# Optimization experiments

Measured on AMD Instinct MI355X. Metric: run time of the kernel, lower is better.

The kernel has to match this reference:

```python
import jax, jax.numpy as jnp
import numpy as np

NUM_HEADS = 8
EPS = 1e-3

N_TOKENS = 32768
DIM = 256
N_WIN = 128
WIN = N_TOKENS // N_WIN  # 256 tokens per window


def setup_inputs() -> dict:
    key = jax.random.key(0)
    ks = jax.random.split(key, 4)
    x = jax.random.normal(ks[0], (N_TOKENS, DIM), dtype=jnp.float32)
    # torch nn.Linear weights are [out_features, in_features]
    w_qkv = jax.random.normal(ks[1], (3 * DIM, DIM), dtype=jnp.float32) * (DIM ** -0.5)
    w_proj = jax.random.normal(ks[2], (DIM, DIM), dtype=jnp.float32) * (DIM ** -0.5)
    b_proj = jnp.zeros((DIM,), dtype=jnp.float32)
    batch_win_inds = (jnp.arange(N_TOKENS) // WIN).astype(jnp.int64)
    offsets = (jnp.arange(N_WIN) * WIN).astype(jnp.int64)
    counts = jnp.full((N_WIN,), WIN, dtype=jnp.int64)
    return {"x": x, "w_qkv": w_qkv, "w_proj": w_proj, "b_proj": b_proj,
            "offsets": offsets, "counts": counts, "batch_win_inds": batch_win_inds}


def reference(x, w_qkv, w_proj, b_proj, offsets, counts, batch_win_inds):
    N, C = x.shape
    H = NUM_HEADS
    hd = C // H
    W = counts.shape[0]  # number of windows (static)

    qkv = x @ w_qkv.T                      # [N, 3C]
    q, k, v = jnp.split(qkv, 3, axis=-1)   # each [N, C]
    q = jax.nn.relu(q.reshape(N, H, hd))   # [N, H, hd]
    k = jax.nn.relu(k.reshape(N, H, hd))
    v = v.reshape(N, H, hd)

    seg = batch_win_inds.astype(jnp.int32)
    # per-window KV state: kv[w] = sum_{i in w} k_i^T v_i   -> [W, H, hd, hd]
    kv = jax.ops.segment_sum(jnp.einsum('nhc,nhd->nhcd', k, v), seg, num_segments=W)
    # per-window key sum for normalizer                      -> [W, H, hd]
    s = jax.ops.segment_sum(k, seg, num_segments=W)

    y = jnp.einsum('nhc,nhcd->nhd', q, kv[seg])              # [N, H, hd]
    z = jnp.sum(s[seg] * q, axis=-1, keepdims=True)          # [N, H, 1]
    y = y / (z + EPS)

    y = y.reshape(N, C) @ w_proj.T + b_proj                  # [N, C]
    return y
```

## Files before the change

### kernel.cpp

```cpp
#include <hip/hip_runtime.h>

typedef __bf16 bf16_t;
typedef bf16_t bf16x8 __attribute__((ext_vector_type(8)));
typedef bf16_t bf16x4 __attribute__((ext_vector_type(4)));
typedef float f32x4 __attribute__((ext_vector_type(4)));

#define M_TOK 32768
#define NWIN 128
#define WIN  256

typedef __attribute__((address_space(3))) void* as3p;
typedef const __attribute__((address_space(1))) void* as1p;

__device__ __forceinline__ void gll16(const void* g, void* l) {
    __builtin_amdgcn_global_load_lds((as1p)g, (as3p)l, 16, 0, 0);
}

__device__ __forceinline__ bf16x8 cvt8(f32x4 a, f32x4 b) {
    bf16x8 o;
    o[0] = (bf16_t)a[0]; o[1] = (bf16_t)a[1]; o[2] = (bf16_t)a[2]; o[3] = (bf16_t)a[3];
    o[4] = (bf16_t)b[0]; o[5] = (bf16_t)b[1]; o[6] = (bf16_t)b[2]; o[7] = (bf16_t)b[3];
    return o;
}

__global__ __launch_bounds__(256) void wconv(
    const float* __restrict__ wq, const float* __restrict__ wp,
    bf16_t* __restrict__ wqb, bf16_t* __restrict__ wpb)
{
    int i4 = (blockIdx.x * 256 + threadIdx.x) * 4;
    const float* s; bf16_t* dst; int idx;
    if (i4 < 196608) { s = wq; dst = wqb; idx = i4; }
    else             { s = wp; dst = wpb; idx = i4 - 196608; }
    f32x4 v = *(const f32x4*)(s + idx);
    bf16x4 o;
    o[0] = (bf16_t)v[0]; o[1] = (bf16_t)v[1]; o[2] = (bf16_t)v[2]; o[3] = (bf16_t)v[3];
    *(bf16x4*)(dst + idx) = o;
}

__global__ __launch_bounds__(256) void gemm1_qkv(
    const float* __restrict__ X,
    const bf16_t* __restrict__ Wb,
    bf16_t* __restrict__ Qg,
    bf16_t* __restrict__ KTg,
    bf16_t* __restrict__ VTg)
{
    __shared__ float  As[4][128][16];
    __shared__ bf16_t Bs[2][128][32];

    const int tid = threadIdx.x;
    const int lane = tid & 63;
    const int wv = tid >> 6;
    const int wm = wv >> 1, wn = wv & 1;
    const int id = blockIdx.x;
    const int sg = id / 48, wsub = id % 48;
    const int m0 = (sg * 8 + (wsub & 7)) * 128;
    const int n0 = (wsub >> 3) * 128;
    const int r = lane & 15, q = lane >> 4;
    const int srow = lane >> 2;

    f32x4 acc[4][4] = {};

    for (int kc = 0; kc < 256; kc += 64) {
#pragma unroll
        for (int p = 0; p < 4; ++p)
#pragma unroll
            for (int g = 0; g < 2; ++g) {
                const int rb = wv * 32 + g * 16;
                gll16(X + (size_t)(m0 + rb + srow) * 256 + kc + p * 16 + (lane & 3) * 4,
                      &As[p][rb][0]);
            }
#pragma unroll
        for (int p = 0; p < 2; ++p)
#pragma unroll
            for (int g = 0; g < 2; ++g) {
                const int rb = wv * 32 + g * 16;
                gll16(Wb + (size_t)(n0 + rb + srow) * 256 + kc + p * 32 + (lane & 3) * 8,
                      &Bs[p][rb][0]);
            }
        __syncthreads();

#pragma unroll
        for (int kk = 0; kk < 64; kk += 32) {
            const int kq = kk + q * 8;
            const int pA = kq >> 4, offA = kq & 15;
            const int pB = kk >> 5;
            bf16x8 a[4], b[4];
#pragma unroll
            for (int i = 0; i < 4; ++i) {
                f32x4 lo = *(const f32x4*)&As[pA][wm * 64 + i * 16 + r][offA];
                f32x4 hi = *(const f32x4*)&As[pA][wm * 64 + i * 16 + r][offA + 4];
                a[i] = cvt8(lo, hi);
            }
#pragma unroll
            for (int j = 0; j < 4; ++j)
                b[j] = *(const bf16x8*)&Bs[pB][wn * 64 + j * 16 + r][q * 8];
#pragma unroll
            for (int i = 0; i < 4; ++i)
#pragma unroll
                for (int j = 0; j < 4; ++j)
                    acc[i][j] = __builtin_amdgcn_mfma_f32_16x16x32_bf16(b[j], a[i], acc[i][j], 0, 0, 0);
        }
        __syncthreads();
    }

#pragma unroll
    for (int i = 0; i < 4; ++i) {
        const int rowg = m0 + wm * 64 + i * 16 + r;
#pragma unroll
        for (int j = 0; j < 4; ++j) {
            const int nbase = n0 + wn * 64 + j * 16 + q * 4;
            if (nbase < 256) {
                const int hq = nbase >> 5, d = nbase & 31;
                bf16x4 o;
#pragma unroll
                for (int reg = 0; reg < 4; ++reg)
                    o[reg] = (bf16_t)fmaxf(acc[i][j][reg], 0.0f);
                *(bf16x4*)&Qg[((size_t)hq * M_TOK + rowg) * 32 + d] = o;
            } else if (nbase < 512) {
                const int hh = (nbase >> 5) - 8, c0 = nbase & 31;
#pragma unroll
                for (int reg = 0; reg < 4; ++reg)
                    KTg[((size_t)hh * 32 + c0 + reg) * M_TOK + rowg] =
                        (bf16_t)fmaxf(acc[i][j][reg], 0.0f);
            } else {
                const int hh = (nbase >> 5) - 16, c0 = nbase & 31;
#pragma unroll
                for (int reg = 0; reg < 4; ++reg)
                    VTg[((size_t)hh * 32 + c0 + reg) * M_TOK + rowg] =
                        (bf16_t)acc[i][j][reg];
            }
        }
    }
}

__global__ __launch_bounds__(256) void gemm2_proj(
    const bf16_t* __restrict__ Y,
    const bf16_t* __restrict__ Wb,
    const float* __restrict__ bias,
    float* __restrict__ Out)
{
    __shared__ bf16_t As[2][128][32];
    __shared__ bf16_t Bs[2][128][32];

    const int tid = threadIdx.x;
    const int lane = tid & 63;
    const int wv = tid >> 6;
    const int wm = wv >> 1, wn = wv & 1;
    const int id = blockIdx.x;
    const int sg = id / 32, wsub = id % 32;
    const int m0 = (sg * 16 + (wsub & 15)) * 128;
    const int n0 = (wsub >> 4) * 128;
    const int r = lane & 15, q = lane >> 4;
    const int srow = lane >> 2;

    f32x4 acc[4][4] = {};

    for (int kc = 0; kc < 256; kc += 64) {
#pragma unroll
        for (int p = 0; p < 2; ++p)
#pragma unroll
            for (int g = 0; g < 2; ++g) {
                const int rb = wv * 32 + g * 16;
                gll16(Y + (size_t)(m0 + rb + srow) * 256 + kc + p * 32 + (lane & 3) * 8,
                      &As[p][rb][0]);
                gll16(Wb + (size_t)(n0 + rb + srow) * 256 + kc + p * 32 + (lane & 3) * 8,
                      &Bs[p][rb][0]);
            }
        __syncthreads();

#pragma unroll
        for (int kk = 0; kk < 64; kk += 32) {
            const int pB = kk >> 5;
            bf16x8 a[4], b[4];
#pragma unroll
            for (int i = 0; i < 4; ++i)
                a[i] = *(const bf16x8*)&As[pB][wm * 64 + i * 16 + r][q * 8];
#pragma unroll
            for (int j = 0; j < 4; ++j)
                b[j] = *(const bf16x8*)&Bs[pB][wn * 64 + j * 16 + r][q * 8];
#pragma unroll
            for (int i = 0; i < 4; ++i)
#pragma unroll
                for (int j = 0; j < 4; ++j)
                    acc[i][j] = __builtin_amdgcn_mfma_f32_16x16x32_bf16(b[j], a[i], acc[i][j], 0, 0, 0);
        }
        __syncthreads();
    }

#pragma unroll
    for (int i = 0; i < 4; ++i) {
        const int rowg = m0 + wm * 64 + i * 16 + r;
#pragma unroll
        for (int j = 0; j < 4; ++j) {
            const int nb = n0 + wn * 64 + j * 16 + q * 4;
            f32x4 bi = *(const f32x4*)(bias + nb);
            f32x4 o;
#pragma unroll
            for (int reg = 0; reg < 4; ++reg) o[reg] = acc[i][j][reg] + bi[reg];
            *(f32x4*)&Out[(size_t)rowg * 256 + nb] = o;
        }
    }
}

__global__ __launch_bounds__(256) void kvy_kernel(
    const bf16_t* __restrict__ Qg,
    const bf16_t* __restrict__ KTg,
    const bf16_t* __restrict__ VTg,
    const int* __restrict__ offsets,
    const int* __restrict__ counts,
    bf16_t* __restrict__ Y)
{
    const int w = blockIdx.x;
    const int h = blockIdx.y;
    const int is64 = (counts[1] == 0) ? 1 : 0;
    const int off = offsets[w << is64];
    const int tid = threadIdx.x;
    const int lane = tid & 63;
    const int wv = tid >> 6;
    const int r = lane & 15, q = lane >> 4;

    __shared__ __align__(16) bf16_t KVT[32 * 40];
    __shared__ float sbuf[32];
    __shared__ float zinv[WIN];

    {
        const int i = wv >> 1, j = wv & 1;
        bf16x8 ones;
#pragma unroll
        for (int u = 0; u < 8; ++u) ones[u] = (bf16_t)1.0f;
        f32x4 acc = {}, accs = {};
        const bf16_t* kr = KTg + ((size_t)h * 32 + i * 16 + r) * M_TOK + off + q * 8;
        const bf16_t* vr = VTg + ((size_t)h * 32 + j * 16 + r) * M_TOK + off + q * 8;
#pragma unroll
        for (int ch = 0; ch < 8; ++ch) {
            bf16x8 af = *(const bf16x8*)(kr + ch * 32);
            bf16x8 bf_ = *(const bf16x8*)(vr + ch * 32);
            acc  = __builtin_amdgcn_mfma_f32_16x16x32_bf16(af, bf_, acc, 0, 0, 0);
            accs = __builtin_amdgcn_mfma_f32_16x16x32_bf16(af, ones, accs, 0, 0, 0);
        }
        bf16x4 kv4;
#pragma unroll
        for (int reg = 0; reg < 4; ++reg) kv4[reg] = (bf16_t)acc[reg];
        *(bf16x4*)(&KVT[(j * 16 + r) * 40 + i * 16 + q * 4]) = kv4;
        if (j == 0 && r == 0) {
#pragma unroll
            for (int reg = 0; reg < 4; ++reg)
                sbuf[i * 16 + q * 4 + reg] = accs[reg];
        }
    }
    __syncthreads();

    {
        const int t = tid;
        const bf16_t* qp = Qg + ((size_t)h * M_TOK + off + t) * 32;
        float z = 0.f;
#pragma unroll
        for (int u = 0; u < 4; ++u) {
            bf16x8 qq = *(const bf16x8*)(qp + u * 8);
#pragma unroll
            for (int jj = 0; jj < 8; ++jj) z += (float)qq[jj] * sbuf[u * 8 + jj];
        }
        zinv[t] = 1.0f / (z + 1e-3f);
    }
    __syncthreads();

    {
        bf16x8 b0 = *(const bf16x8*)(&KVT[(r) * 40 + q * 8]);
        bf16x8 b1 = *(const bf16x8*)(&KVT[(16 + r) * 40 + q * 8]);
#pragma unroll
        for (int u = 0; u < 4; ++u) {
            const int mi = wv * 4 + u;
            const bf16_t* ap = Qg + ((size_t)h * M_TOK + off + mi * 16 + r) * 32 + q * 8;
            bf16x8 af = *(const bf16x8*)ap;
            f32x4 acc0 = {}, acc1 = {};
            acc0 = __builtin_amdgcn_mfma_f32_16x16x32_bf16(b0, af, acc0, 0, 0, 0);
            acc1 = __builtin_amdgcn_mfma_f32_16x16x32_bf16(b1, af, acc1, 0, 0, 0);
            const int tkn = mi * 16 + r;
            const float zi = zinv[tkn];
            bf16_t* yp = Y + (size_t)(off + tkn) * 256 + h * 32;
            bf16x4 o0, o1;
#pragma unroll
            for (int reg = 0; reg < 4; ++reg) {
                o0[reg] = (bf16_t)(acc0[reg] * zi);
                o1[reg] = (bf16_t)(acc1[reg] * zi);
            }
            *(bf16x4*)(yp + q * 4) = o0;
            *(bf16x4*)(yp + 16 + q * 4) = o1;
        }
    }
}

extern "C" void kernel_launch(void* const* d_in, const int* in_sizes, int n_in,
                              void* d_out, int out_size, void* d_ws, size_t ws_size,
                              hipStream_t stream) {
    const float* x      = (const float*)d_in[0];
    const float* w_qkv  = (const float*)d_in[1];
    const float* w_proj = (const float*)d_in[2];
    const float* b_proj = (const float*)d_in[3];
    const int*   offs   = (const int*)d_in[4];
    const int*   cnts   = (const int*)d_in[5];

    char* ws = (char*)d_ws;
    bf16_t* Qg  = (bf16_t*)ws;
    bf16_t* KTg = (bf16_t*)(ws + 16777216);
    bf16_t* VTg = (bf16_t*)(ws + 33554432);
    bf16_t* Y   = (bf16_t*)(ws + 50331648);
    bf16_t* Wqb = (bf16_t*)(ws + 67108864);
    bf16_t* Wpb = (bf16_t*)(ws + 67502080);
    float*  out = (float*)d_out;

    wconv<<<256, 256, 0, stream>>>(w_qkv, w_proj, Wqb, Wpb);

    gemm1_qkv<<<1536, 256, 0, stream>>>(x, Wqb, Qg, KTg, VTg);

    kvy_kernel<<<dim3(NWIN, 8), 256, 0, stream>>>(Qg, KTg, VTg, offs, cnts, Y);

    gemm2_proj<<<512, 256, 0, stream>>>(Y, Wpb, b_proj, out);
}
```

Before: 146.2 us.

## Swap MFMA operands for K/V tiles to vectorize transposed stores; shrink proj tiles

```diff
diff --git a/kernel.cpp b/kernel.cpp
--- a/kernel.cpp
+++ b/kernel.cpp
@@ -57,6 +57,7 @@
     const int n0 = (wsub >> 3) * 128;
     const int r = lane & 15, q = lane >> 4;
     const int srow = lane >> 2;
+    const bool qblk = (n0 < 256);
 
     f32x4 acc[4][4] = {};
 
@@ -94,40 +95,57 @@
 #pragma unroll
             for (int j = 0; j < 4; ++j)
                 b[j] = *(const bf16x8*)&Bs[pB][wn * 64 + j * 16 + r][q * 8];
-#pragma unroll
-            for (int i = 0; i < 4; ++i)
-#pragma unroll
-                for (int j = 0; j < 4; ++j)
-                    acc[i][j] = __builtin_amdgcn_mfma_f32_16x16x32_bf16(b[j], a[i], acc[i][j], 0, 0, 0);
+            if (qblk) {
+#pragma unroll
+                for (int i = 0; i < 4; ++i)
+#pragma unroll
+                    for (int j = 0; j < 4; ++j)
+                        acc[i][j] = __builtin_amdgcn_mfma_f32_16x16x32_bf16(b[j], a[i], acc[i][j], 0, 0, 0);
+            } else {
+#pragma unroll
+                for (int i = 0; i < 4; ++i)
+#pragma unroll
+                    for (int j = 0; j < 4; ++j)
+                        acc[i][j] = __builtin_amdgcn_mfma_f32_16x16x32_bf16(a[i], b[j], acc[i][j], 0, 0, 0);
+            }
         }
         __syncthreads();
     }
 
-#pragma unroll
-    for (int i = 0; i < 4; ++i) {
-        const int rowg = m0 + wm * 64 + i * 16 + r;
-#pragma unroll
-        for (int j = 0; j < 4; ++j) {
-            const int nbase = n0 + wn * 64 + j * 16 + q * 4;
-            if (nbase < 256) {
-                const int hq = nbase >> 5, d = nbase & 31;
+    if (qblk) {
+#pragma unroll
+        for (int i = 0; i < 4; ++i) {
+            const int rowg = m0 + wm * 64 + i * 16 + r;
+#pragma unroll
+            for (int j = 0; j < 4; ++j) {
+                const int nb = n0 + wn * 64 + j * 16 + q * 4;
+                const int hq = nb >> 5, d = nb & 31;
                 bf16x4 o;
 #pragma unroll
                 for (int reg = 0; reg < 4; ++reg)
                     o[reg] = (bf16_t)fmaxf(acc[i][j][reg], 0.0f);
                 *(bf16x4*)&Qg[((size_t)hq * M_TOK + rowg) * 32 + d] = o;
-            } else if (nbase < 512) {
-                const int hh = (nbase >> 5) - 8, c0 = nbase & 31;
-#pragma unroll
-                for (int reg = 0; reg < 4; ++reg)
-                    KTg[((size_t)hh * 32 + c0 + reg) * M_TOK + rowg] =
-                        (bf16_t)fmaxf(acc[i][j][reg], 0.0f);
-            } else {
-                const int hh = (nbase >> 5) - 16, c0 = nbase & 31;
-#pragma unroll
-                for (int reg = 0; reg < 4; ++reg)
-                    VTg[((size_t)hh * 32 + c0 + reg) * M_TOK + rowg] =
-                        (bf16_t)acc[i][j][reg];
+            }
+        }
+    } else {
+        const bool isK = (n0 < 512);
+        bf16_t* base = isK ? KTg : VTg;
+#pragma unroll
+        for (int i = 0; i < 4; ++i) {
+            const int tok0 = m0 + wm * 64 + i * 16 + q * 4;
+#pragma unroll
+            for (int j = 0; j < 4; ++j) {
+                const int nb = n0 + wn * 64 + j * 16 + r;
+                const int hh = (nb >> 5) & 7;
+                const int c  = nb & 31;
+                bf16x4 o;
+#pragma unroll
+                for (int reg = 0; reg < 4; ++reg) {
+                    float v = acc[i][j][reg];
+                    if (isK) v = fmaxf(v, 0.0f);
+                    o[reg] = (bf16_t)v;
+                }
+                *(bf16x4*)&base[((size_t)hh * 32 + c) * M_TOK + tok0] = o;
             }
         }
     }
@@ -139,49 +157,48 @@
     const float* __restrict__ bias,
     float* __restrict__ Out)
 {
-    __shared__ bf16_t As[2][128][32];
+    __shared__ bf16_t As[2][64][32];
     __shared__ bf16_t Bs[2][128][32];
 
     const int tid = threadIdx.x;
     const int lane = tid & 63;
     const int wv = tid >> 6;
-    const int wm = wv >> 1, wn = wv & 1;
     const int id = blockIdx.x;
-    const int sg = id / 32, wsub = id % 32;
-    const int m0 = (sg * 16 + (wsub & 15)) * 128;
-    const int n0 = (wsub >> 4) * 128;
+    const int sg = id / 16, wsub = id % 16;
+    const int m0 = (sg * 8 + (wsub & 7)) * 64;
+    const int n0 = (wsub >> 3) * 128;
     const int r = lane & 15, q = lane >> 4;
     const int srow = lane >> 2;
 
-    f32x4 acc[4][4] = {};
+    f32x4 acc[4][2] = {};
 
     for (int kc = 0; kc < 256; kc += 64) {
 #pragma unroll
         for (int p = 0; p < 2; ++p)
-#pragma unroll
-            for (int g = 0; g < 2; ++g) {
-                const int rb = wv * 32 + g * 16;
-                gll16(Y + (size_t)(m0 + rb + srow) * 256 + kc + p * 32 + (lane & 3) * 8,
-                      &As[p][rb][0]);
-                gll16(Wb + (size_t)(n0 + rb + srow) * 256 + kc + p * 32 + (lane & 3) * 8,
-                      &Bs[p][rb][0]);
-            }
+            gll16(Y + (size_t)(m0 + wv * 16 + srow) * 256 + kc + p * 32 + (lane & 3) * 8,
+                  &As[p][wv * 16][0]);
+#pragma unroll
+        for (int p = 0; p < 2; ++p)
+#pragma unroll
+            for (int g = 0; g < 2; ++g)
+                gll16(Wb + (size_t)(n0 + wv * 32 + g * 16 + srow) * 256 + kc + p * 32 + (lane & 3) * 8,
+                      &Bs[p][wv * 32 + g * 16][0]);
         __syncthreads();
 
 #pragma unroll
         for (int kk = 0; kk < 64; kk += 32) {
             const int pB = kk >> 5;
-            bf16x8 a[4], b[4];
+            bf16x8 a[4], b[2];
 #pragma unroll
             for (int i = 0; i < 4; ++i)
-                a[i] = *(const bf16x8*)&As[pB][wm * 64 + i * 16 + r][q * 8];
-#pragma unroll
-            for (int j = 0; j < 4; ++j)
-                b[j] = *(const bf16x8*)&Bs[pB][wn * 64 + j * 16 + r][q * 8];
+                a[i] = *(const bf16x8*)&As[pB][i * 16 + r][q * 8];
+#pragma unroll
+            for (int j = 0; j < 2; ++j)
+                b[j] = *(const bf16x8*)&Bs[pB][wv * 32 + j * 16 + r][q * 8];
 #pragma unroll
             for (int i = 0; i < 4; ++i)
 #pragma unroll
-                for (int j = 0; j < 4; ++j)
+                for (int j = 0; j < 2; ++j)
                     acc[i][j] = __builtin_amdgcn_mfma_f32_16x16x32_bf16(b[j], a[i], acc[i][j], 0, 0, 0);
         }
         __syncthreads();
@@ -189,10 +206,10 @@
 
 #pragma unroll
     for (int i = 0; i < 4; ++i) {
-        const int rowg = m0 + wm * 64 + i * 16 + r;
-#pragma unroll
-        for (int j = 0; j < 4; ++j) {
-            const int nb = n0 + wn * 64 + j * 16 + q * 4;
+        const int rowg = m0 + i * 16 + r;
+#pragma unroll
+        for (int j = 0; j < 2; ++j) {
+            const int nb = n0 + wv * 32 + j * 16 + q * 4;
             f32x4 bi = *(const f32x4*)(bias + nb);
             f32x4 o;
 #pragma unroll
@@ -315,5 +332,5 @@
 
     kvy_kernel<<<dim3(NWIN, 8), 256, 0, stream>>>(Qg, KTg, VTg, offs, cnts, Y);
 
-    gemm2_proj<<<512, 256, 0, stream>>>(Y, Wpb, b_proj, out);
-}
+    gemm2_proj<<<1024, 256, 0, stream>>>(Y, Wpb, b_proj, out);
+}
```

Measured after the change: 164.6 us. +12.6%, slower.
